# Kernel optimization log

Hardware: AMD Instinct MI355X
Metric: run time of the kernel (lower is better)

## Reference

```python
import jax, jax.numpy as jnp
import numpy as np

N = 50000
E = 800000
G = 256          # number of graphs in the batch
F_IN = 128
H1, D1 = 12, 32  # conv1: heads, out-per-head (concat -> 384)
H2, D2 = 1, 64   # conv2: single head
NEG_SLOPE = 0.2


def setup_inputs() -> dict:
    key = jax.random.key(0)
    ks = jax.random.split(key, 12)
    x = jax.random.normal(ks[0], (N, F_IN), dtype=jnp.float32)
    edge_index = jax.random.randint(ks[1], (2, E), 0, N, dtype=jnp.int64)
    batch = jnp.sort(jax.random.randint(ks[2], (N,), 0, G, dtype=jnp.int64))
    # conv1 params (Glorot-ish scaling)
    W1 = jax.random.normal(ks[3], (F_IN, H1 * D1), dtype=jnp.float32) * (1.0 / np.sqrt(F_IN))
    att_src1 = jax.random.normal(ks[4], (H1, D1), dtype=jnp.float32) * (1.0 / np.sqrt(D1))
    att_dst1 = jax.random.normal(ks[5], (H1, D1), dtype=jnp.float32) * (1.0 / np.sqrt(D1))
    bias1 = jnp.zeros((H1 * D1,), dtype=jnp.float32)
    # conv2 params
    W2 = jax.random.normal(ks[6], (H1 * D1, H2 * D2), dtype=jnp.float32) * (1.0 / np.sqrt(H1 * D1))
    att_src2 = jax.random.normal(ks[7], (H2, D2), dtype=jnp.float32) * (1.0 / np.sqrt(D2))
    att_dst2 = jax.random.normal(ks[8], (H2, D2), dtype=jnp.float32) * (1.0 / np.sqrt(D2))
    bias2 = jnp.zeros((H2 * D2,), dtype=jnp.float32)
    return {"x": x, "edge_index": edge_index, "batch": batch,
            "W1": W1, "att_src1": att_src1, "att_dst1": att_dst1, "bias1": bias1,
            "W2": W2, "att_src2": att_src2, "att_dst2": att_dst2, "bias2": bias2}


def gat_conv(x, src, dst, W, att_src, att_dst, bias, heads, d_out):
    # x: [N, F] -> h: [N, heads, d_out]
    h = (x @ W).reshape(N, heads, d_out)
    # per-node attention halves: [N, heads]
    a_src = jnp.einsum('nhd,hd->nh', h, att_src)
    a_dst = jnp.einsum('nhd,hd->nh', h, att_dst)
    # per-edge logits (edges include self-loops): [Etot, heads]
    e = jax.nn.leaky_relu(a_src[src] + a_dst[dst], NEG_SLOPE)
    # segment softmax over incoming edges of each destination node
    m = jax.ops.segment_max(e, dst, num_segments=N)          # [N, heads]
    e = jnp.exp(e - m[dst])
    s = jax.ops.segment_sum(e, dst, num_segments=N)          # [N, heads]
    alpha = e / s[dst]
    # weighted aggregation: [N, heads, d_out]
    out = jax.ops.segment_sum(alpha[:, :, None] * h[src], dst, num_segments=N)
    return out.reshape(N, heads * d_out) + bias


def reference(x, edge_index, batch, W1, att_src1, att_dst1, bias1,
              W2, att_src2, att_dst2, bias2):
    # add self-loops (PyG GATConv default add_self_loops=True)
    loops = jnp.arange(N, dtype=edge_index.dtype)
    src = jnp.concatenate([edge_index[0], loops])
    dst = jnp.concatenate([edge_index[1], loops])

    h = jax.nn.relu(gat_conv(x, src, dst, W1, att_src1, att_dst1, bias1, H1, D1))
    h = gat_conv(h, src, dst, W2, att_src2, att_dst2, bias2, H2, D2)

    # global mean pool over graphs
    sums = jax.ops.segment_sum(h, batch, num_segments=G)                 # [G, 64]
    cnts = jax.ops.segment_sum(jnp.ones((N,), h.dtype), batch, num_segments=G)
    return sums / jnp.maximum(cnts, 1.0)[:, None]
```

## Files before the change

kernel.cpp:

```cpp
#include <hip/hip_runtime.h>

#define N_NODES 50000
#define N_EDGES 800000
#define ETOT (N_EDGES + N_NODES)
#define G_GRAPHS 256
#define F_IN 128
#define H1 12
#define D1 32
#define C1 (H1*D1)
#define C2 64
#define NEG 0.2f
#define SCAN_B 1024
#define NBLK_SCAN ((N_NODES + SCAN_B - 1)/SCAN_B)

using bf16x8  = __attribute__((ext_vector_type(8))) short;
using ushort8 = __attribute__((ext_vector_type(8))) unsigned short;
using f32x4   = __attribute__((ext_vector_type(4))) float;

__device__ __forceinline__ float lrelu(float x){ return x > 0.f ? x : NEG*x; }
__device__ __forceinline__ unsigned short f2bf(float f){
  unsigned u = __float_as_uint(f);
  u += 0x7fffu + ((u >> 16) & 1u);
  return (unsigned short)(u >> 16);
}
__device__ __forceinline__ float bf2f(unsigned short h){
  return __uint_as_float(((unsigned)h) << 16);
}

__global__ void cast_x_kernel(const float* __restrict__ x, unsigned short* __restrict__ xb){
  int i = blockIdx.x*blockDim.x + threadIdx.x;
  int base = i*4;
  if (base >= N_NODES*F_IN) return;
  float4 v = *(const float4*)(x + base);
  ushort4 o; o.x=f2bf(v.x); o.y=f2bf(v.y); o.z=f2bf(v.z); o.w=f2bf(v.w);
  *(ushort4*)(xb + base) = o;
}
__global__ void transpose_w_kernel(const float* __restrict__ W, unsigned short* __restrict__ Wt,
                                   int K, int Nc){
  int i = blockIdx.x*blockDim.x + threadIdx.x;
  if (i >= K*Nc) return;
  int n = i / K, k = i % K;
  Wt[i] = f2bf(W[(size_t)k*Nc + n]);
}
__global__ void wab_prep(const float* __restrict__ W1, const float* __restrict__ att_src,
                         const float* __restrict__ att_dst, unsigned short* __restrict__ wAb){
  int i = blockIdx.x*blockDim.x + threadIdx.x;
  if (i >= 32*F_IN) return;
  int c = i >> 7, k = i & 127;
  float v = 0.f;
  if (c < 12){
    #pragma unroll
    for (int dd=0; dd<D1; ++dd) v += W1[(size_t)k*C1 + c*D1 + dd] * att_src[c*D1 + dd];
  } else if (c < 24){
    int h = c - 12;
    #pragma unroll
    for (int dd=0; dd<D1; ++dd) v += W1[(size_t)k*C1 + h*D1 + dd] * att_dst[h*D1 + dd];
  }
  wAb[i] = f2bf(v);
}

template<int BM,int BN,int WM,int WN,bool F32OUT>
__global__ __launch_bounds__(256) void gemm_mfma(const unsigned short* __restrict__ A,
    const unsigned short* __restrict__ Bt, void* __restrict__ Cv,
    int M, int N, int K){
  constexpr int BK = 32;
  __shared__ unsigned short As2[4][BM][8];
  __shared__ unsigned short Bs2[4][BN][8];
  const int tid  = threadIdx.x;
  const int wid  = tid >> 6, lane = tid & 63;
  constexpr int NWX = BN / WN;
  const int wrow = (wid / NWX) * WM, wcol = (wid % NWX) * WN;
  constexpr int MR = WM/16, NR = WN/16;
  const int row0 = blockIdx.x * BM, col0 = blockIdx.y * BN;
  const int r = lane & 15, koct = lane >> 4;
  f32x4 acc[MR][NR];
  #pragma unroll
  for (int m=0;m<MR;m++)
    #pragma unroll
    for (int n=0;n<NR;n++) acc[m][n] = f32x4{0.f,0.f,0.f,0.f};

  for (int k0 = 0; k0 < K; k0 += BK){
    for (int s = tid; s < BM*8; s += 256){
      int rr = s >> 3, cc = (s & 7) * 4;
      int gr = row0 + rr;
      ushort4 v = (gr < M) ? *(const ushort4*)(A + (size_t)gr*K + k0 + cc)
                           : ushort4{0,0,0,0};
      *(ushort4*)(&As2[cc>>3][rr][cc&7]) = v;
    }
    for (int s = tid; s < BN*8; s += 256){
      int rr = s >> 3, cc = (s & 7) * 4;
      ushort4 v = *(const ushort4*)(Bt + (size_t)(col0+rr)*K + k0 + cc);
      *(ushort4*)(&Bs2[cc>>3][rr][cc&7]) = v;
    }
    __syncthreads();
    bf16x8 af[MR], bq[NR];
    #pragma unroll
    for (int m=0;m<MR;m++) af[m] = *(const bf16x8*)(&As2[koct][wrow + m*16 + r][0]);
    #pragma unroll
    for (int n=0;n<NR;n++) bq[n] = *(const bf16x8*)(&Bs2[koct][wcol + n*16 + r][0]);
    #pragma unroll
    for (int m=0;m<MR;m++)
      #pragma unroll
      for (int n=0;n<NR;n++)
        acc[m][n] = __builtin_amdgcn_mfma_f32_16x16x32_bf16(af[m], bq[n], acc[m][n], 0,0,0);
    __syncthreads();
  }
  #pragma unroll
  for (int m=0;m<MR;m++){
    #pragma unroll
    for (int rr=0; rr<4; rr++){
      int grow = row0 + wrow + m*16 + koct*4 + rr;
      if (grow < M){
        #pragma unroll
        for (int n=0;n<NR;n++){
          if constexpr (F32OUT)
            ((float*)Cv)[(size_t)grow*N + col0 + wcol + n*16 + r] = acc[m][n][rr];
          else
            ((unsigned short*)Cv)[(size_t)grow*N + col0 + wcol + n*16 + r] = f2bf(acc[m][n][rr]);
        }
      }
    }
  }
}

__global__ void count_kernel(const int* __restrict__ ei, int* __restrict__ counts){
  int e = blockIdx.x*blockDim.x + threadIdx.x;
  if (e >= ETOT) return;
  int d = (e < N_EDGES) ? ei[N_EDGES + e] : (e - N_EDGES);
  atomicAdd(&counts[d], 1);
}
__global__ __launch_bounds__(SCAN_B) void scan_pass1(const int* __restrict__ counts,
    int* __restrict__ excl, int* __restrict__ bsum){
  __shared__ int sdata[SCAN_B];
  int i = blockIdx.x*SCAN_B + threadIdx.x;
  int v = (i < N_NODES) ? counts[i] : 0;
  sdata[threadIdx.x] = v;
  __syncthreads();
  for (int off=1; off<SCAN_B; off<<=1){
    int t = (threadIdx.x >= off) ? sdata[threadIdx.x-off] : 0;
    __syncthreads();
    sdata[threadIdx.x] += t;
    __syncthreads();
  }
  if (i < N_NODES) excl[i] = sdata[threadIdx.x] - v;
  if (threadIdx.x == SCAN_B-1) bsum[blockIdx.x] = sdata[SCAN_B-1];
}
__global__ void scan_pass2(int* __restrict__ bsum){
  if (threadIdx.x == 0){
    int acc = 0;
    for (int b=0;b<NBLK_SCAN;b++){ int t = bsum[b]; bsum[b] = acc; acc += t; }
  }
}
__global__ void scan_pass3(int* __restrict__ rowptr, const int* __restrict__ bsum,
                           int* __restrict__ cursor){
  int i = blockIdx.x*blockDim.x + threadIdx.x;
  if (i < N_NODES){
    int r = rowptr[i] + bsum[i/SCAN_B];
    rowptr[i] = r; cursor[i] = r;
  }
  if (i == N_NODES) rowptr[N_NODES] = ETOT;
}
__global__ void scatter_kernel(const int* __restrict__ ei, int* __restrict__ cursor,
                               int* __restrict__ csr_src){
  int e = blockIdx.x*blockDim.x + threadIdx.x;
  if (e >= ETOT) return;
  int s, d;
  if (e < N_EDGES){ s = ei[e]; d = ei[N_EDGES + e]; } else { s = d = e - N_EDGES; }
  int slot = atomicAdd(&cursor[d], 1);
  csr_src[slot] = s;
}

__global__ __launch_bounds__(256) void alpha1_kernel(const int* __restrict__ rowptr,
    const int* __restrict__ csr, const float* __restrict__ asd,
    float* __restrict__ alpha){
  int d = blockIdx.x*4 + (threadIdx.x >> 6);
  int lane = threadIdx.x & 63;
  int r0 = rowptr[d], r1 = rowptr[d+1], deg = r1 - r0;
  float4 ad0 = *(const float4*)(asd + (size_t)d*32 + 12);
  float4 ad1 = *(const float4*)(asd + (size_t)d*32 + 16);
  float4 ad2 = *(const float4*)(asd + (size_t)d*32 + 20);
  float ad[12] = {ad0.x,ad0.y,ad0.z,ad0.w, ad1.x,ad1.y,ad1.z,ad1.w, ad2.x,ad2.y,ad2.z,ad2.w};

  if (deg <= 64){
    bool act = lane < deg;
    int j = r0 + lane;
    int s = act ? csr[j] : 0;
    float4 s0 = *(const float4*)(asd + (size_t)s*32);
    float4 s1 = *(const float4*)(asd + (size_t)s*32 + 4);
    float4 s2 = *(const float4*)(asd + (size_t)s*32 + 8);
    float as[12] = {s0.x,s0.y,s0.z,s0.w, s1.x,s1.y,s1.z,s1.w, s2.x,s2.y,s2.z,s2.w};
    float w[12];
    #pragma unroll
    for (int h=0; h<12; ++h){
      float l = act ? lrelu(as[h] + ad[h]) : -1e30f;
      float m = l;
      #pragma unroll
      for (int off=32; off; off>>=1) m = fmaxf(m, __shfl_xor(m, off));
      float wv = act ? __expf(l - m) : 0.f;
      float ss = wv;
      #pragma unroll
      for (int off=32; off; off>>=1) ss += __shfl_xor(ss, off);
      w[h] = wv / ss;
    }
    if (act){
      *(float4*)(alpha + (size_t)j*12)     = float4{w[0],w[1],w[2],w[3]};
      *(float4*)(alpha + (size_t)j*12 + 4) = float4{w[4],w[5],w[6],w[7]};
      *(float4*)(alpha + (size_t)j*12 + 8) = float4{w[8],w[9],w[10],w[11]};
    }
  } else {
    float mx[12], ss[12];
    #pragma unroll
    for (int h=0;h<12;h++){ mx[h] = -1e30f; ss[h] = 0.f; }
    for (int j = r0 + lane; j < r1; j += 64){
      int s = csr[j];
      float4 s0 = *(const float4*)(asd + (size_t)s*32);
      float4 s1 = *(const float4*)(asd + (size_t)s*32 + 4);
      float4 s2 = *(const float4*)(asd + (size_t)s*32 + 8);
      float as[12] = {s0.x,s0.y,s0.z,s0.w, s1.x,s1.y,s1.z,s1.w, s2.x,s2.y,s2.z,s2.w};
      #pragma unroll
      for (int h=0;h<12;h++) mx[h] = fmaxf(mx[h], lrelu(as[h] + ad[h]));
    }
    #pragma unroll
    for (int h=0;h<12;h++){
      #pragma unroll
      for (int off=32; off; off>>=1) mx[h] = fmaxf(mx[h], __shfl_xor(mx[h], off));
    }
    for (int j = r0 + lane; j < r1; j += 64){
      int s = csr[j];
      float4 s0 = *(const float4*)(asd + (size_t)s*32);
      float4 s1 = *(const float4*)(asd + (size_t)s*32 + 4);
      float4 s2 = *(const float4*)(asd + (size_t)s*32 + 8);
      float as[12] = {s0.x,s0.y,s0.z,s0.w, s1.x,s1.y,s1.z,s1.w, s2.x,s2.y,s2.z,s2.w};
      float w[12];
      #pragma unroll
      for (int h=0;h<12;h++){ w[h] = __expf(lrelu(as[h]+ad[h]) - mx[h]); ss[h] += w[h]; }
      *(float4*)(alpha + (size_t)j*12)     = float4{w[0],w[1],w[2],w[3]};
      *(float4*)(alpha + (size_t)j*12 + 4) = float4{w[4],w[5],w[6],w[7]};
      *(float4*)(alpha + (size_t)j*12 + 8) = float4{w[8],w[9],w[10],w[11]};
    }
    float inv[12];
    #pragma unroll
    for (int h=0;h<12;h++){
      #pragma unroll
      for (int off=32; off; off>>=1) ss[h] += __shfl_xor(ss[h], off);
      inv[h] = 1.f / ss[h];
    }
    for (int j = r0 + lane; j < r1; j += 64){
      float4 o0 = *(const float4*)(alpha + (size_t)j*12);
      float4 o1 = *(const float4*)(alpha + (size_t)j*12 + 4);
      float4 o2 = *(const float4*)(alpha + (size_t)j*12 + 8);
      o0.x*=inv[0]; o0.y*=inv[1]; o0.z*=inv[2]; o0.w*=inv[3];
      o1.x*=inv[4]; o1.y*=inv[5]; o1.z*=inv[6]; o1.w*=inv[7];
      o2.x*=inv[8]; o2.y*=inv[9]; o2.z*=inv[10]; o2.w*=inv[11];
      *(float4*)(alpha + (size_t)j*12)     = o0;
      *(float4*)(alpha + (size_t)j*12 + 4) = o1;
      *(float4*)(alpha + (size_t)j*12 + 8) = o2;
    }
  }
}

__global__ __launch_bounds__(256) void agg1c_kernel(const int* __restrict__ rowptr,
    const int* __restrict__ csr, const unsigned short* __restrict__ xb,
    const float* __restrict__ alpha, const unsigned short* __restrict__ w1t,
    const float* __restrict__ bias, unsigned short* __restrict__ out1){
  constexpr int ROWE = 6*F_IN + 8;
  constexpr int WROW = 16*12 + 4;
  __shared__ unsigned short agg[16*ROWE];
  __shared__ float wlds[16][WROW];

  const int tid  = threadIdx.x;
  const int slot = tid >> 4;
  const int t16  = tid & 15;
  const int base = ((tid & 63) >> 4) * 16;
  const int d    = blockIdx.x*16 + slot;
  const int r0 = rowptr[d], r1 = rowptr[d+1];

  float acc[12][8];
  #pragma unroll
  for (int h=0;h<12;h++)
    #pragma unroll
    for (int i=0;i<8;i++) acc[h][i] = 0.f;

  for (int c0 = r0; c0 < r1; c0 += 16){
    int nc = min(16, r1 - c0);
    int s_st = 0;
    if (t16 < nc){
      int j = c0 + t16;
      s_st = csr[j];
      float4 a0 = *(const float4*)(alpha + (size_t)j*12);
      float4 a1 = *(const float4*)(alpha + (size_t)j*12 + 4);
      float4 a2 = *(const float4*)(alpha + (size_t)j*12 + 8);
      *(float4*)(&wlds[slot][t16*12 + 0]) = a0;
      *(float4*)(&wlds[slot][t16*12 + 4]) = a1;
      *(float4*)(&wlds[slot][t16*12 + 8]) = a2;
    }
    __builtin_amdgcn_wave_barrier();
    int sA = __shfl(s_st, base + 0);
    ushort8 xA = *(const ushort8*)(xb + (size_t)sA*F_IN + t16*8);
    ushort8 xB = {0,0,0,0,0,0,0,0};
    if (nc > 1){
      int sB = __shfl(s_st, base + 1);
      xB = *(const ushort8*)(xb + (size_t)sB*F_IN + t16*8);
    }
    for (int e = 0; e < nc; ++e){
      ushort8 cx = xA;
      xA = xB;
      if (e + 2 < nc){
        int sN = __shfl(s_st, base + e + 2);
        xB = *(const ushort8*)(xb + (size_t)sN*F_IN + t16*8);
      }
      float4 w0 = *(const float4*)(&wlds[slot][e*12 + 0]);
      float4 w1 = *(const float4*)(&wlds[slot][e*12 + 4]);
      float4 w2 = *(const float4*)(&wlds[slot][e*12 + 8]);
      float xf[8];
      #pragma unroll
      for (int i=0;i<8;i++) xf[i] = bf2f((unsigned short)cx[i]);
      float w[12] = {w0.x,w0.y,w0.z,w0.w, w1.x,w1.y,w1.z,w1.w, w2.x,w2.y,w2.z,w2.w};
      #pragma unroll
      for (int h=0;h<12;h++)
        #pragma unroll
        for (int i=0;i<8;i++) acc[h][i] += w[h]*xf[i];
    }
    __builtin_amdgcn_wave_barrier();
  }

  const int wv = tid >> 6, lane = tid & 63;
  const int er = lane & 15, eq = lane >> 4;
  #pragma unroll
  for (int hf = 0; hf < 2; ++hf){
    __syncthreads();
    #pragma unroll
    for (int h = 0; h < 6; ++h){
      int hh = hf*6 + h;
      ushort8 v;
      #pragma unroll
      for (int i=0;i<8;i++) v[i] = f2bf(acc[hh][i]);
      *(ushort8*)(&agg[slot*ROWE + h*F_IN + t16*8]) = v;
    }
    __syncthreads();
    for (int tt = wv; tt < 12; tt += 4){
      int h = tt >> 1, nb = tt & 1;
      int hh = hf*6 + h;
      f32x4 c = {0.f,0.f,0.f,0.f};
      #pragma unroll
      for (int kk=0; kk<4; ++kk){
        bf16x8 af = *(const bf16x8*)(&agg[er*ROWE + h*F_IN + kk*32 + eq*8]);
        bf16x8 bq = *(const bf16x8*)(w1t + (size_t)(hh*32 + nb*16 + er)*F_IN + kk*32 + eq*8);
        c = __builtin_amdgcn_mfma_f32_16x16x32_bf16(af, bq, c, 0,0,0);
      }
      int col = hh*32 + nb*16 + er;
      float bv = bias[col];
      #pragma unroll
      for (int rr=0; rr<4; ++rr){
        int od = blockIdx.x*16 + eq*4 + rr;
        out1[(size_t)od*C1 + col] = f2bf(fmaxf(c[rr] + bv, 0.f));
      }
    }
  }
}

__global__ void a2_kernel(const unsigned short* __restrict__ h2,
    const float* __restrict__ att_src, const float* __restrict__ att_dst,
    float* __restrict__ a_src, float* __restrict__ a_dst){
  int n = blockIdx.x*blockDim.x + threadIdx.x;
  if (n >= N_NODES) return;
  const unsigned short* hp = h2 + (size_t)n*C2;
  float s=0.f, d=0.f;
  #pragma unroll
  for (int k4=0;k4<16;k4++){
    ushort4 v = *(const ushort4*)(hp + k4*4);
    int b = k4*4;
    s += bf2f(v.x)*att_src[b] + bf2f(v.y)*att_src[b+1] + bf2f(v.z)*att_src[b+2] + bf2f(v.w)*att_src[b+3];
    d += bf2f(v.x)*att_dst[b] + bf2f(v.y)*att_dst[b+1] + bf2f(v.z)*att_dst[b+2] + bf2f(v.w)*att_dst[b+3];
  }
  a_src[n]=s; a_dst[n]=d;
}

__global__ __launch_bounds__(256) void agg2c_kernel(const int* __restrict__ rowptr,
    const int* __restrict__ csr, const unsigned short* __restrict__ h2,
    const float* __restrict__ asrc, const float* __restrict__ adst,
    const float* __restrict__ bias, const int* __restrict__ batch,
    float* __restrict__ pool){
  const int tid  = threadIdx.x;
  const int slot = tid >> 4;
  const int t16  = tid & 15;
  const int base = ((tid & 63) >> 4) * 16;
  const int d    = blockIdx.x*16 + slot;
  const int r0 = rowptr[d], r1 = rowptr[d+1];
  const float ad = adst[d];

  float m = -1e30f, ss = 0.f;
  float a0=0.f, a1=0.f, a2=0.f, a3=0.f;

  for (int c0 = r0; c0 < r1; c0 += 16){
    int nc = min(16, r1 - c0);
    int s_st = 0; float al_st = 0.f;
    if (t16 < nc){
      s_st = csr[c0 + t16];
      al_st = asrc[s_st];
    }
    int sA = __shfl(s_st, base + 0);
    ushort4 xA = *(const ushort4*)(h2 + (size_t)sA*C2 + t16*4);
    ushort4 xB = {0,0,0,0};
    if (nc > 1){
      int sB = __shfl(s_st, base + 1);
      xB = *(const ushort4*)(h2 + (size_t)sB*C2 + t16*4);
    }
    for (int e = 0; e < nc; ++e){
      ushort4 cx = xA;
      xA = xB;
      if (e + 2 < nc){
        int sN = __shfl(s_st, base + e + 2);
        xB = *(const ushort4*)(h2 + (size_t)sN*C2 + t16*4);
      }
      float a = __shfl(al_st, base + e);
      float l = lrelu(a + ad);
      float mn = fmaxf(m, l);
      float corr = __expf(m - mn);
      float w = __expf(l - mn);
      ss = ss*corr + w;
      a0 = a0*corr + w*bf2f(cx.x);
      a1 = a1*corr + w*bf2f(cx.y);
      a2 = a2*corr + w*bf2f(cx.z);
      a3 = a3*corr + w*bf2f(cx.w);
      m = mn;
    }
  }
  float inv = 1.f / ss;
  int g = batch[d];
  int fb = t16*4;
  atomicAdd(&pool[g*C2 + fb+0], a0*inv + bias[fb+0]);
  atomicAdd(&pool[g*C2 + fb+1], a1*inv + bias[fb+1]);
  atomicAdd(&pool[g*C2 + fb+2], a2*inv + bias[fb+2]);
  atomicAdd(&pool[g*C2 + fb+3], a3*inv + bias[fb+3]);
}

__global__ void cnt_kernel(const int* __restrict__ batch, int* __restrict__ cnt){
  int n = blockIdx.x*blockDim.x + threadIdx.x;
  if (n < N_NODES) atomicAdd(&cnt[batch[n]], 1);
}
__global__ void finalize_kernel(const float* __restrict__ sums, const int* __restrict__ cnt,
                                float* __restrict__ out){
  int i = blockIdx.x*blockDim.x + threadIdx.x;
  if (i >= G_GRAPHS*C2) return;
  int g = i >> 6;
  out[i] = sums[i] / fmaxf((float)cnt[g], 1.f);
}

extern "C" void kernel_launch(void* const* d_in, const int* in_sizes, int n_in,
                              void* d_out, int out_size, void* d_ws, size_t ws_size,
                              hipStream_t stream) {
  const float* x        = (const float*)d_in[0];
  const int*   ei       = (const int*)  d_in[1];
  const int*   batch    = (const int*)  d_in[2];
  const float* W1       = (const float*)d_in[3];
  const float* att_src1 = (const float*)d_in[4];
  const float* att_dst1 = (const float*)d_in[5];
  const float* bias1    = (const float*)d_in[6];
  const float* W2       = (const float*)d_in[7];
  const float* att_src2 = (const float*)d_in[8];
  const float* att_dst2 = (const float*)d_in[9];
  const float* bias2    = (const float*)d_in[10];
  float* out = (float*)d_out;

  char* ws = (char*)d_ws;
  size_t o = 0;
  auto alloc = [&](size_t bytes)->size_t{ size_t r=o; o=(o+bytes+255)&~(size_t)255; return r; };

  size_t xb_o     = alloc((size_t)N_NODES*F_IN*2);
  size_t w1t_o    = alloc((size_t)C1*F_IN*2);
  size_t w2t_o    = alloc((size_t)C2*C1*2);
  size_t wab_o    = alloc((size_t)32*F_IN*2);
  size_t asd_o    = alloc((size_t)N_NODES*32*4);
  size_t out1_o   = alloc((size_t)N_NODES*C1*2);
  size_t h2_o     = alloc((size_t)N_NODES*C2*2);
  size_t asrc2_o  = alloc((size_t)N_NODES*4);
  size_t adst2_o  = alloc((size_t)N_NODES*4);
  size_t alpha1_o = alloc((size_t)ETOT*H1*4);
  size_t zero_beg = o;
  size_t counts_o = alloc((size_t)N_NODES*4);
  size_t pool_o   = alloc((size_t)G_GRAPHS*C2*4);
  size_t cnt_o    = alloc((size_t)G_GRAPHS*4);
  size_t zero_end = o;
  size_t rowptr_o = alloc((size_t)(N_NODES+1)*4);
  size_t bsum_o   = alloc((size_t)NBLK_SCAN*4);
  size_t cursor_o = alloc((size_t)N_NODES*4);
  size_t csr_o    = alloc((size_t)ETOT*4);

  unsigned short* xb    = (unsigned short*)(ws + xb_o);
  unsigned short* w1t   = (unsigned short*)(ws + w1t_o);
  unsigned short* w2t   = (unsigned short*)(ws + w2t_o);
  unsigned short* wab   = (unsigned short*)(ws + wab_o);
  float* asd    = (float*)(ws + asd_o);
  unsigned short* out1b = (unsigned short*)(ws + out1_o);
  unsigned short* h2b   = (unsigned short*)(ws + h2_o);
  float* asrc2  = (float*)(ws + asrc2_o);
  float* adst2  = (float*)(ws + adst2_o);
  float* alpha1 = (float*)(ws + alpha1_o);
  int*   counts = (int*)  (ws + counts_o);
  float* poolf  = (float*)(ws + pool_o);
  int*   cnt    = (int*)  (ws + cnt_o);
  int*   rowptr = (int*)  (ws + rowptr_o);
  int*   bsum   = (int*)  (ws + bsum_o);
  int*   cursor = (int*)  (ws + cursor_o);
  int*   csrsrc = (int*)  (ws + csr_o);

  hipMemsetAsync(ws + zero_beg, 0, zero_end - zero_beg, stream);

  const int TPB = 256;
  int egrid = (ETOT + TPB - 1)/TPB;

  cast_x_kernel<<<(N_NODES*F_IN/4 + TPB-1)/TPB, TPB, 0, stream>>>(x, xb);
  transpose_w_kernel<<<(F_IN*C1 + TPB-1)/TPB, TPB, 0, stream>>>(W1, w1t, F_IN, C1);
  transpose_w_kernel<<<(C1*C2 + TPB-1)/TPB, TPB, 0, stream>>>(W2, w2t, C1, C2);
  wab_prep<<<(32*F_IN + TPB-1)/TPB, TPB, 0, stream>>>(W1, att_src1, att_dst1, wab);

  count_kernel<<<egrid, TPB, 0, stream>>>(ei, counts);
  scan_pass1<<<NBLK_SCAN, SCAN_B, 0, stream>>>(counts, rowptr, bsum);
  scan_pass2<<<1, 64, 0, stream>>>(bsum);
  scan_pass3<<<(N_NODES + TPB)/TPB, TPB, 0, stream>>>(rowptr, bsum, cursor);
  scatter_kernel<<<egrid, TPB, 0, stream>>>(ei, cursor, csrsrc);

  gemm_mfma<64,32,32,16,true><<<dim3((N_NODES+63)/64, 1), 256, 0, stream>>>(xb, wab, asd, N_NODES, 32, F_IN);
  alpha1_kernel<<<(N_NODES+3)/4, 256, 0, stream>>>(rowptr, csrsrc, asd, alpha1);
  agg1c_kernel<<<N_NODES/16, 256, 0, stream>>>(rowptr, csrsrc, xb, alpha1, w1t, bias1, out1b);

  gemm_mfma<64,64,32,32,false><<<dim3((N_NODES+63)/64, 1), 256, 0, stream>>>(out1b, w2t, h2b, N_NODES, C2, C1);
  a2_kernel<<<(N_NODES + TPB-1)/TPB, TPB, 0, stream>>>(h2b, att_src2, att_dst2, asrc2, adst2);
  agg2c_kernel<<<(N_NODES+15)/16, 256, 0, stream>>>(rowptr, csrsrc, h2b, asrc2, adst2, bias2, batch, poolf);

  cnt_kernel<<<(N_NODES + TPB-1)/TPB, TPB, 0, stream>>>(batch, cnt);
  finalize_kernel<<<(G_GRAPHS*C2 + TPB-1)/TPB, TPB, 0, stream>>>(poolf, cnt, out);
}
```

Before: 469.1 us.

## Fuse attention softmax into layer-1 aggregation and merge small prep kernels

Removes the separate alpha1 kernel and its per-edge alpha buffer. Unnormalized exp weights are now computed inline in the layer-1 aggregation, which uses 512 threads with two half-waves per node, each covering six heads, and normalizes once at the end. Layer 2 drops the online-softmax rescaling and instead sums clamped exps, then divides. The prep, count and scan kernels are merged to reduce launches. Skipping max subtraction relies on a clamp at 30 to avoid overflow, so it can lose accuracy when logits are large, and the larger block raises register pressure.

```diff
diff --git a/kernel.cpp b/kernel.cpp
--- a/kernel.cpp
+++ b/kernel.cpp
@@ -26,37 +26,49 @@
 __device__ __forceinline__ float bf2f(unsigned short h){
   return __uint_as_float(((unsigned)h) << 16);
 }
-
-__global__ void cast_x_kernel(const float* __restrict__ x, unsigned short* __restrict__ xb){
-  int i = blockIdx.x*blockDim.x + threadIdx.x;
-  int base = i*4;
-  if (base >= N_NODES*F_IN) return;
-  float4 v = *(const float4*)(x + base);
-  ushort4 o; o.x=f2bf(v.x); o.y=f2bf(v.y); o.z=f2bf(v.z); o.w=f2bf(v.w);
-  *(ushort4*)(xb + base) = o;
-}
-__global__ void transpose_w_kernel(const float* __restrict__ W, unsigned short* __restrict__ Wt,
-                                   int K, int Nc){
-  int i = blockIdx.x*blockDim.x + threadIdx.x;
-  if (i >= K*Nc) return;
-  int n = i / K, k = i % K;
-  Wt[i] = f2bf(W[(size_t)k*Nc + n]);
-}
-__global__ void wab_prep(const float* __restrict__ W1, const float* __restrict__ att_src,
-                         const float* __restrict__ att_dst, unsigned short* __restrict__ wAb){
-  int i = blockIdx.x*blockDim.x + threadIdx.x;
-  if (i >= 32*F_IN) return;
-  int c = i >> 7, k = i & 127;
-  float v = 0.f;
-  if (c < 12){
-    #pragma unroll
-    for (int dd=0; dd<D1; ++dd) v += W1[(size_t)k*C1 + c*D1 + dd] * att_src[c*D1 + dd];
-  } else if (c < 24){
-    int h = c - 12;
-    #pragma unroll
-    for (int dd=0; dd<D1; ++dd) v += W1[(size_t)k*C1 + h*D1 + dd] * att_dst[h*D1 + dd];
-  }
-  wAb[i] = f2bf(v);
+__device__ __forceinline__ float wexp(float l){ return __expf(fminf(l, 30.f)); }
+
+#define B_CAST ((N_NODES*F_IN/4 + 255)/256)
+#define B_W1   ((F_IN*C1 + 255)/256)
+#define B_W2   ((C1*C2 + 255)/256)
+#define B_WAB  ((32*F_IN + 255)/256)
+__global__ void prep_kernel(const float* __restrict__ x, const float* __restrict__ W1,
+    const float* __restrict__ W2, const float* __restrict__ att_src,
+    const float* __restrict__ att_dst, unsigned short* __restrict__ xb,
+    unsigned short* __restrict__ w1t, unsigned short* __restrict__ w2t,
+    unsigned short* __restrict__ wAb){
+  int b = blockIdx.x, tid = threadIdx.x;
+  if (b < B_CAST){
+    int base = (b*256 + tid)*4;
+    if (base >= N_NODES*F_IN) return;
+    float4 v = *(const float4*)(x + base);
+    ushort4 o; o.x=f2bf(v.x); o.y=f2bf(v.y); o.z=f2bf(v.z); o.w=f2bf(v.w);
+    *(ushort4*)(xb + base) = o;
+  } else if (b < B_CAST + B_W1){
+    int i = (b - B_CAST)*256 + tid;
+    if (i >= F_IN*C1) return;
+    int n = i / F_IN, k = i % F_IN;
+    w1t[i] = f2bf(W1[(size_t)k*C1 + n]);
+  } else if (b < B_CAST + B_W1 + B_W2){
+    int i = (b - B_CAST - B_W1)*256 + tid;
+    if (i >= C1*C2) return;
+    int n = i / C1, k = i % C1;
+    w2t[i] = f2bf(W2[(size_t)k*C2 + n]);
+  } else {
+    int i = (b - B_CAST - B_W1 - B_W2)*256 + tid;
+    if (i >= 32*F_IN) return;
+    int c = i >> 7, k = i & 127;
+    float v = 0.f;
+    if (c < 12){
+      #pragma unroll
+      for (int dd=0; dd<D1; ++dd) v += W1[(size_t)k*C1 + c*D1 + dd] * att_src[c*D1 + dd];
+    } else if (c < 24){
+      int h = c - 12;
+      #pragma unroll
+      for (int dd=0; dd<D1; ++dd) v += W1[(size_t)k*C1 + h*D1 + dd] * att_dst[h*D1 + dd];
+    }
+    wAb[i] = f2bf(v);
+  }
 }
 
 template<int BM,int BN,int WM,int WN,bool F32OUT>
@@ -123,11 +135,19 @@
   }
 }
 
-__global__ void count_kernel(const int* __restrict__ ei, int* __restrict__ counts){
-  int e = blockIdx.x*blockDim.x + threadIdx.x;
-  if (e >= ETOT) return;
-  int d = (e < N_EDGES) ? ei[N_EDGES + e] : (e - N_EDGES);
-  atomicAdd(&counts[d], 1);
+#define EGRID ((ETOT + 255)/256)
+#define NGRID ((N_NODES + 255)/256)
+__global__ void count_cnt_kernel(const int* __restrict__ ei, const int* __restrict__ batch,
+                                 int* __restrict__ counts, int* __restrict__ cnt){
+  if ((int)blockIdx.x < EGRID){
+    int e = blockIdx.x*256 + threadIdx.x;
+    if (e >= ETOT) return;
+    int d = (e < N_EDGES) ? ei[N_EDGES + e] : (e - N_EDGES);
+    atomicAdd(&counts[d], 1);
+  } else {
+    int n = (blockIdx.x - EGRID)*256 + threadIdx.x;
+    if (n < N_NODES) atomicAdd(&cnt[batch[n]], 1);
+  }
 }
 __global__ __launch_bounds__(SCAN_B) void scan_pass1(const int* __restrict__ counts,
     int* __restrict__ excl, int* __restrict__ bsum){
@@ -145,17 +165,19 @@
   if (i < N_NODES) excl[i] = sdata[threadIdx.x] - v;
   if (threadIdx.x == SCAN_B-1) bsum[blockIdx.x] = sdata[SCAN_B-1];
 }
-__global__ void scan_pass2(int* __restrict__ bsum){
-  if (threadIdx.x == 0){
-    int acc = 0;
-    for (int b=0;b<NBLK_SCAN;b++){ int t = bsum[b]; bsum[b] = acc; acc += t; }
-  }
-}
 __global__ void scan_pass3(int* __restrict__ rowptr, const int* __restrict__ bsum,
                            int* __restrict__ cursor){
-  int i = blockIdx.x*blockDim.x + threadIdx.x;
+  __shared__ int carry_s;
+  int sblk = blockIdx.x >> 2;
+  if (threadIdx.x == 0){
+    int c = 0;
+    for (int b=0; b<sblk; ++b) c += bsum[b];
+    carry_s = c;
+  }
+  __syncthreads();
+  int i = blockIdx.x*256 + (int)threadIdx.x;
   if (i < N_NODES){
-    int r = rowptr[i] + bsum[i/SCAN_B];
+    int r = rowptr[i] + carry_s;
     rowptr[i] = r; cursor[i] = r;
   }
   if (i == N_NODES) rowptr[N_NODES] = ETOT;
@@ -170,175 +192,110 @@
   csr_src[slot] = s;
 }
 
-__global__ __launch_bounds__(256) void alpha1_kernel(const int* __restrict__ rowptr,
-    const int* __restrict__ csr, const float* __restrict__ asd,
-    float* __restrict__ alpha){
-  int d = blockIdx.x*4 + (threadIdx.x >> 6);
-  int lane = threadIdx.x & 63;
-  int r0 = rowptr[d], r1 = rowptr[d+1], deg = r1 - r0;
+__global__ __launch_bounds__(512) void agg1s_kernel(const int* __restrict__ rowptr,
+    const int* __restrict__ csr, const unsigned short* __restrict__ xb,
+    const float* __restrict__ asd, const unsigned short* __restrict__ w1t,
+    const float* __restrict__ bias, unsigned short* __restrict__ out1){
+  constexpr int ROWE = 6*F_IN + 8;
+  constexpr int WROW = 32*12 + 4;
+  __shared__ unsigned short agg[16*ROWE];
+  __shared__ float wlds[16][WROW];
+
+  const int tid    = threadIdx.x;
+  const int slot   = tid >> 5;
+  const int lane32 = tid & 31;
+  const int h16    = lane32 >> 4;
+  const int t16    = lane32 & 15;
+  const int gbase  = tid & 32;
+  const int d      = blockIdx.x*16 + slot;
+  const int r0 = rowptr[d], r1 = rowptr[d+1];
+
   float4 ad0 = *(const float4*)(asd + (size_t)d*32 + 12);
   float4 ad1 = *(const float4*)(asd + (size_t)d*32 + 16);
   float4 ad2 = *(const float4*)(asd + (size_t)d*32 + 20);
   float ad[12] = {ad0.x,ad0.y,ad0.z,ad0.w, ad1.x,ad1.y,ad1.z,ad1.w, ad2.x,ad2.y,ad2.z,ad2.w};
 
-  if (deg <= 64){
-    bool act = lane < deg;
-    int j = r0 + lane;
-    int s = act ? csr[j] : 0;
-    float4 s0 = *(const float4*)(asd + (size_t)s*32);
-    float4 s1 = *(const float4*)(asd + (size_t)s*32 + 4);
-    float4 s2 = *(const float4*)(asd + (size_t)s*32 + 8);
-    float as[12] = {s0.x,s0.y,s0.z,s0.w, s1.x,s1.y,s1.z,s1.w, s2.x,s2.y,s2.z,s2.w};
-    float w[12];
-    #pragma unroll
-    for (int h=0; h<12; ++h){
-      float l = act ? lrelu(as[h] + ad[h]) : -1e30f;
-      float m = l;
-      #pragma unroll
-      for (int off=32; off; off>>=1) m = fmaxf(m, __shfl_xor(m, off));
-      float wv = act ? __expf(l - m) : 0.f;
-      float ss = wv;
-      #pragma unroll
-      for (int off=32; off; off>>=1) ss += __shfl_xor(ss, off);
-      w[h] = wv / ss;
-    }
-    if (act){
-      *(float4*)(alpha + (size_t)j*12)     = float4{w[0],w[1],w[2],w[3]};
-      *(float4*)(alpha + (size_t)j*12 + 4) = float4{w[4],w[5],w[6],w[7]};
-      *(float4*)(alpha + (size_t)j*12 + 8) = float4{w[8],w[9],w[10],w[11]};
-    }
-  } else {
-    float mx[12], ss[12];
-    #pragma unroll
-    for (int h=0;h<12;h++){ mx[h] = -1e30f; ss[h] = 0.f; }
-    for (int j = r0 + lane; j < r1; j += 64){
-      int s = csr[j];
-      float4 s0 = *(const float4*)(asd + (size_t)s*32);
-      float4 s1 = *(const float4*)(asd + (size_t)s*32 + 4);
-      float4 s2 = *(const float4*)(asd + (size_t)s*32 + 8);
-      float as[12] = {s0.x,s0.y,s0.z,s0.w, s1.x,s1.y,s1.z,s1.w, s2.x,s2.y,s2.z,s2.w};
-      #pragma unroll
-      for (int h=0;h<12;h++) mx[h] = fmaxf(mx[h], lrelu(as[h] + ad[h]));
-    }
-    #pragma unroll
-    for (int h=0;h<12;h++){
-      #pragma unroll
-      for (int off=32; off; off>>=1) mx[h] = fmaxf(mx[h], __shfl_xor(mx[h], off));
-    }
-    for (int j = r0 + lane; j < r1; j += 64){
-      int s = csr[j];
-      float4 s0 = *(const float4*)(asd + (size_t)s*32);
-      float4 s1 = *(const float4*)(asd + (size_t)s*32 + 4);
-      float4 s2 = *(const float4*)(asd + (size_t)s*32 + 8);
+  float acc[6][8];
+  #pragma unroll
+  for (int h=0;h<6;h++)
+    #pragma unroll
+    for (int i=0;i<8;i++) acc[h][i] = 0.f;
+  float ss[12];
+  #pragma unroll
+  for (int h=0;h<12;h++) ss[h] = 0.f;
+
+  for (int c0 = r0; c0 < r1; c0 += 32){
+    int nc = min(32, r1 - c0);
+    int s_st = 0;
+    if (lane32 < nc){
+      int j = c0 + lane32;
+      s_st = csr[j];
+      float4 s0 = *(const float4*)(asd + (size_t)s_st*32);
+      float4 s1 = *(const float4*)(asd + (size_t)s_st*32 + 4);
+      float4 s2 = *(const float4*)(asd + (size_t)s_st*32 + 8);
       float as[12] = {s0.x,s0.y,s0.z,s0.w, s1.x,s1.y,s1.z,s1.w, s2.x,s2.y,s2.z,s2.w};
       float w[12];
       #pragma unroll
-      for (int h=0;h<12;h++){ w[h] = __expf(lrelu(as[h]+ad[h]) - mx[h]); ss[h] += w[h]; }
-      *(float4*)(alpha + (size_t)j*12)     = float4{w[0],w[1],w[2],w[3]};
-      *(float4*)(alpha + (size_t)j*12 + 4) = float4{w[4],w[5],w[6],w[7]};
-      *(float4*)(alpha + (size_t)j*12 + 8) = float4{w[8],w[9],w[10],w[11]};
-    }
-    float inv[12];
-    #pragma unroll
-    for (int h=0;h<12;h++){
-      #pragma unroll
-      for (int off=32; off; off>>=1) ss[h] += __shfl_xor(ss[h], off);
-      inv[h] = 1.f / ss[h];
-    }
-    for (int j = r0 + lane; j < r1; j += 64){
-      float4 o0 = *(const float4*)(alpha + (size_t)j*12);
-      float4 o1 = *(const float4*)(alpha + (size_t)j*12 + 4);
-      float4 o2 = *(const float4*)(alpha + (size_t)j*12 + 8);
-      o0.x*=inv[0]; o0.y*=inv[1]; o0.z*=inv[2]; o0.w*=inv[3];
-      o1.x*=inv[4]; o1.y*=inv[5]; o1.z*=inv[6]; o1.w*=inv[7];
-      o2.x*=inv[8]; o2.y*=inv[9]; o2.z*=inv[10]; o2.w*=inv[11];
-      *(float4*)(alpha + (size_t)j*12)     = o0;
-      *(float4*)(alpha + (size_t)j*12 + 4) = o1;
-      *(float4*)(alpha + (size_t)j*12 + 8) = o2;
-    }
-  }
-}
-
-__global__ __launch_bounds__(256) void agg1c_kernel(const int* __restrict__ rowptr,
-    const int* __restrict__ csr, const unsigned short* __restrict__ xb,
-    const float* __restrict__ alpha, const unsigned short* __restrict__ w1t,
-    const float* __restrict__ bias, unsigned short* __restrict__ out1){
-  constexpr int ROWE = 6*F_IN + 8;
-  constexpr int WROW = 16*12 + 4;
-  __shared__ unsigned short agg[16*ROWE];
-  __shared__ float wlds[16][WROW];
-
-  const int tid  = threadIdx.x;
-  const int slot = tid >> 4;
-  const int t16  = tid & 15;
-  const int base = ((tid & 63) >> 4) * 16;
-  const int d    = blockIdx.x*16 + slot;
-  const int r0 = rowptr[d], r1 = rowptr[d+1];
-
-  float acc[12][8];
-  #pragma unroll
-  for (int h=0;h<12;h++)
-    #pragma unroll
-    for (int i=0;i<8;i++) acc[h][i] = 0.f;
-
-  for (int c0 = r0; c0 < r1; c0 += 16){
-    int nc = min(16, r1 - c0);
-    int s_st = 0;
-    if (t16 < nc){
-      int j = c0 + t16;
-      s_st = csr[j];
-      float4 a0 = *(const float4*)(alpha + (size_t)j*12);
-      float4 a1 = *(const float4*)(alpha + (size_t)j*12 + 4);
-      float4 a2 = *(const float4*)(alpha + (size_t)j*12 + 8);
-      *(float4*)(&wlds[slot][t16*12 + 0]) = a0;
-      *(float4*)(&wlds[slot][t16*12 + 4]) = a1;
-      *(float4*)(&wlds[slot][t16*12 + 8]) = a2;
+      for (int h=0;h<12;h++){ w[h] = wexp(lrelu(as[h] + ad[h])); ss[h] += w[h]; }
+      *(float4*)(&wlds[slot][lane32*12 + 0]) = float4{w[0],w[1],w[2],w[3]};
+      *(float4*)(&wlds[slot][lane32*12 + 4]) = float4{w[4],w[5],w[6],w[7]};
+      *(float4*)(&wlds[slot][lane32*12 + 8]) = float4{w[8],w[9],w[10],w[11]};
     }
     __builtin_amdgcn_wave_barrier();
-    int sA = __shfl(s_st, base + 0);
+    int sA = __shfl(s_st, gbase + 0);
     ushort8 xA = *(const ushort8*)(xb + (size_t)sA*F_IN + t16*8);
     ushort8 xB = {0,0,0,0,0,0,0,0};
     if (nc > 1){
-      int sB = __shfl(s_st, base + 1);
+      int sB = __shfl(s_st, gbase + 1);
       xB = *(const ushort8*)(xb + (size_t)sB*F_IN + t16*8);
     }
     for (int e = 0; e < nc; ++e){
       ushort8 cx = xA;
       xA = xB;
       if (e + 2 < nc){
-        int sN = __shfl(s_st, base + e + 2);
+        int sN = __shfl(s_st, gbase + e + 2);
         xB = *(const ushort8*)(xb + (size_t)sN*F_IN + t16*8);
       }
-      float4 w0 = *(const float4*)(&wlds[slot][e*12 + 0]);
-      float4 w1 = *(const float4*)(&wlds[slot][e*12 + 4]);
-      float4 w2 = *(const float4*)(&wlds[slot][e*12 + 8]);
+      float2 w0 = *(const float2*)(&wlds[slot][e*12 + h16*6 + 0]);
+      float2 w1 = *(const float2*)(&wlds[slot][e*12 + h16*6 + 2]);
+      float2 w2 = *(const float2*)(&wlds[slot][e*12 + h16*6 + 4]);
       float xf[8];
       #pragma unroll
       for (int i=0;i<8;i++) xf[i] = bf2f((unsigned short)cx[i]);
-      float w[12] = {w0.x,w0.y,w0.z,w0.w, w1.x,w1.y,w1.z,w1.w, w2.x,w2.y,w2.z,w2.w};
-      #pragma unroll
-      for (int h=0;h<12;h++)
+      float wv6[6] = {w0.x,w0.y, w1.x,w1.y, w2.x,w2.y};
+      #pragma unroll
+      for (int h=0;h<6;h++)
         #pragma unroll
-        for (int i=0;i<8;i++) acc[h][i] += w[h]*xf[i];
+        for (int i=0;i<8;i++) acc[h][i] += wv6[h]*xf[i];
     }
     __builtin_amdgcn_wave_barrier();
   }
 
-  const int wv = tid >> 6, lane = tid & 63;
-  const int er = lane & 15, eq = lane >> 4;
+  #pragma unroll
+  for (int h=0;h<12;h++){
+    #pragma unroll
+    for (int off=16; off; off>>=1) ss[h] += __shfl_xor(ss[h], off);
+  }
+  float inv[6];
+  #pragma unroll
+  for (int h=0;h<6;h++) inv[h] = 1.f / ss[h16*6 + h];
+
+  const int wv = tid >> 6, wl = tid & 63;
+  const int er = wl & 15, eq = wl >> 4;
   #pragma unroll
   for (int hf = 0; hf < 2; ++hf){
     __syncthreads();
-    #pragma unroll
-    for (int h = 0; h < 6; ++h){
-      int hh = hf*6 + h;
-      ushort8 v;
-      #pragma unroll
-      for (int i=0;i<8;i++) v[i] = f2bf(acc[hh][i]);
-      *(ushort8*)(&agg[slot*ROWE + h*F_IN + t16*8]) = v;
-    }
-    __syncthreads();
-    for (int tt = wv; tt < 12; tt += 4){
+    if (h16 == hf){
+      #pragma unroll
+      for (int h = 0; h < 6; ++h){
+        ushort8 v;
+        #pragma unroll
+        for (int i=0;i<8;i++) v[i] = f2bf(acc[h][i]*inv[h]);
+        *(ushort8*)(&agg[slot*ROWE + h*F_IN + t16*8]) = v;
+      }
+    }
+    __syncthreads();
+    for (int tt = wv; tt < 12; tt += 8){
       int h = tt >> 1, nb = tt & 1;
       int hh = hf*6 + h;
       f32x4 c = {0.f,0.f,0.f,0.f};
@@ -376,7 +333,7 @@
   a_src[n]=s; a_dst[n]=d;
 }
 
-__global__ __launch_bounds__(256) void agg2c_kernel(const int* __restrict__ rowptr,
+__global__ __launch_bounds__(256) void agg2s_kernel(const int* __restrict__ rowptr,
     const int* __restrict__ csr, const unsigned short* __restrict__ h2,
     const float* __restrict__ asrc, const float* __restrict__ adst,
     const float* __restrict__ bias, const int* __restrict__ batch,
@@ -389,15 +346,16 @@
   const int r0 = rowptr[d], r1 = rowptr[d+1];
   const float ad = adst[d];
 
-  float m = -1e30f, ss = 0.f;
+  float ssp = 0.f;
   float a0=0.f, a1=0.f, a2=0.f, a3=0.f;
 
   for (int c0 = r0; c0 < r1; c0 += 16){
     int nc = min(16, r1 - c0);
-    int s_st = 0; float al_st = 0.f;
+    int s_st = 0; float w_st = 0.f;
     if (t16 < nc){
       s_st = csr[c0 + t16];
-      al_st = asrc[s_st];
+      w_st = wexp(lrelu(asrc[s_st] + ad));
+      ssp += w_st;
     }
     int sA = __shfl(s_st, base + 0);
     ushort4 xA = *(const ushort4*)(h2 + (size_t)sA*C2 + t16*4);
@@ -413,20 +371,16 @@
         int sN = __shfl(s_st, base + e + 2);
         xB = *(const ushort4*)(h2 + (size_t)sN*C2 + t16*4);
       }
-      float a = __shfl(al_st, base + e);
-      float l = lrelu(a + ad);
-      float mn = fmaxf(m, l);
-      float corr = __expf(m - mn);
-      float w = __expf(l - mn);
-      ss = ss*corr + w;
-      a0 = a0*corr + w*bf2f(cx.x);
-      a1 = a1*corr + w*bf2f(cx.y);
-      a2 = a2*corr + w*bf2f(cx.z);
-      a3 = a3*corr + w*bf2f(cx.w);
-      m = mn;
-    }
-  }
-  float inv = 1.f / ss;
+      float w = __shfl(w_st, base + e);
+      a0 += w*bf2f(cx.x);
+      a1 += w*bf2f(cx.y);
+      a2 += w*bf2f(cx.z);
+      a3 += w*bf2f(cx.w);
+    }
+  }
+  #pragma unroll
+  for (int off=8; off; off>>=1) ssp += __shfl_xor(ssp, off);
+  float inv = 1.f / ssp;
   int g = batch[d];
   int fb = t16*4;
   atomicAdd(&pool[g*C2 + fb+0], a0*inv + bias[fb+0]);
@@ -435,10 +389,6 @@
   atomicAdd(&pool[g*C2 + fb+3], a3*inv + bias[fb+3]);
 }
 
-__global__ void cnt_kernel(const int* __restrict__ batch, int* __restrict__ cnt){
-  int n = blockIdx.x*blockDim.x + threadIdx.x;
-  if (n < N_NODES) atomicAdd(&cnt[batch[n]], 1);
-}
 __global__ void finalize_kernel(const float* __restrict__ sums, const int* __restrict__ cnt,
                                 float* __restrict__ out){
   int i = blockIdx.x*blockDim.x + threadIdx.x;
@@ -476,7 +426,6 @@
   size_t h2_o     = alloc((size_t)N_NODES*C2*2);
   size_t asrc2_o  = alloc((size_t)N_NODES*4);
   size_t adst2_o  = alloc((size_t)N_NODES*4);
-  size_t alpha1_o = alloc((size_t)ETOT*H1*4);
   size_t zero_beg = o;
   size_t counts_o = alloc((size_t)N_NODES*4);
   size_t pool_o   = alloc((size_t)G_GRAPHS*C2*4);
@@ -496,7 +445,6 @@
   unsigned short* h2b   = (unsigned short*)(ws + h2_o);
   float* asrc2  = (float*)(ws + asrc2_o);
   float* adst2  = (float*)(ws + adst2_o);
-  float* alpha1 = (float*)(ws + alpha1_o);
   int*   counts = (int*)  (ws + counts_o);
   float* poolf  = (float*)(ws + pool_o);
   int*   cnt    = (int*)  (ws + cnt_o);
@@ -508,27 +456,21 @@
   hipMemsetAsync(ws + zero_beg, 0, zero_end - zero_beg, stream);
 
   const int TPB = 256;
-  int egrid = (ETOT + TPB - 1)/TPB;
-
-  cast_x_kernel<<<(N_NODES*F_IN/4 + TPB-1)/TPB, TPB, 0, stream>>>(x, xb);
-  transpose_w_kernel<<<(F_IN*C1 + TPB-1)/TPB, TPB, 0, stream>>>(W1, w1t, F_IN, C1);
-  transpose_w_kernel<<<(C1*C2 + TPB-1)/TPB, TPB, 0, stream>>>(W2, w2t, C1, C2);
-  wab_prep<<<(32*F_IN + TPB-1)/TPB, TPB, 0, stream>>>(W1, att_src1, att_dst1, wab);
-
-  count_kernel<<<egrid, TPB, 0, stream>>>(ei, counts);
+
+  prep_kernel<<<B_CAST + B_W1 + B_W2 + B_WAB, TPB, 0, stream>>>(
+      x, W1, W2, att_src1, att_dst1, xb, w1t, w2t, wab);
+
+  count_cnt_kernel<<<EGRID + NGRID, TPB, 0, stream>>>(ei, batch, counts, cnt);
   scan_pass1<<<NBLK_SCAN, SCAN_B, 0, stream>>>(counts, rowptr, bsum);
-  scan_pass2<<<1, 64, 0, stream>>>(bsum);
-  scan_pass3<<<(N_NODES + TPB)/TPB, TPB, 0, stream>>>(rowptr, bsum, cursor);
-  scatter_kernel<<<egrid, TPB, 0, stream>>>(ei, cursor, csrsrc);
+  scan_pass3<<<(N_NODES + 1 + 255)/256, TPB, 0, stream>>>(rowptr, bsum, cursor);
+  scatter_kernel<<<EGRID, TPB, 0, stream>>>(ei, cursor, csrsrc);
 
   gemm_mfma<64,32,32,16,true><<<dim3((N_NODES+63)/64, 1), 256, 0, stream>>>(xb, wab, asd, N_NODES, 32, F_IN);
-  alpha1_kernel<<<(N_NODES+3)/4, 256, 0, stream>>>(rowptr, csrsrc, asd, alpha1);
-  agg1c_kernel<<<N_NODES/16, 256, 0, stream>>>(rowptr, csrsrc, xb, alpha1, w1t, bias1, out1b);
+  agg1s_kernel<<<N_NODES/16, 512, 0, stream>>>(rowptr, csrsrc, xb, asd, w1t, bias1, out1b);
 
   gemm_mfma<64,64,32,32,false><<<dim3((N_NODES+63)/64, 1), 256, 0, stream>>>(out1b, w2t, h2b, N_NODES, C2, C1);
   a2_kernel<<<(N_NODES + TPB-1)/TPB, TPB, 0, stream>>>(h2b, att_src2, att_dst2, asrc2, adst2);
-  agg2c_kernel<<<(N_NODES+15)/16, 256, 0, stream>>>(rowptr, csrsrc, h2b, asrc2, adst2, bias2, batch, poolf);
-
-  cnt_kernel<<<(N_NODES + TPB-1)/TPB, TPB, 0, stream>>>(batch, cnt);
+  agg2s_kernel<<<(N_NODES+15)/16, TPB, 0, stream>>>(rowptr, csrsrc, h2b, asrc2, adst2, bias2, batch, poolf);
+
   finalize_kernel<<<(G_GRAPHS*C2 + TPB-1)/TPB, TPB, 0, stream>>>(poolf, cnt, out);
 }
```

After: 442.1 us. 5.7% less time.
